# Optimization experiments

Hardware: AMD Instinct MI355X
Metric: run time of the kernel (lower is better)

Reference implementation:

```python
import jax, jax.numpy as jnp
import numpy as np

BS, LS, NWRD, D, H, NTGT, MC = 32, 512, 100000, 128, 512, 2048, 20
TEMP = 0.5  # gumbel-softmax temperature (self.last_t)
HLOSS_COEF = 0.03


def setup_inputs() -> dict:
    key = jax.random.key(0)
    ks = jax.random.split(key, 12)
    inp_word = jax.random.randint(ks[0], (BS, LS), 0, NWRD, dtype=jnp.int32)
    inp_char = jax.random.randint(ks[1], (BS, LS, MC), 0, 95, dtype=jnp.int32)
    inp_pos = jax.random.randint(ks[2], (BS, LS), 0, 50, dtype=jnp.int32)
    keyword_table = jax.random.bernoulli(ks[3], 0.1, (NWRD,))  # wid in keywords_set
    tgt_ids = jax.random.randint(ks[4], (NTGT,), 0, NWRD, dtype=jnp.int32)
    lut = jax.random.randint(ks[5], (NWRD, MC), 0, 95, dtype=jnp.int32)
    u = jax.random.uniform(ks[6], (BS, LS, NTGT), minval=1e-6, maxval=1.0 - 1e-6)
    gumbel = -jnp.log(-jnp.log(u))  # standard Gumbel(0,1) noise
    W = jax.random.normal(ks[7], (NWRD, D), dtype=jnp.float32) * 0.02
    W1 = jax.random.normal(ks[8], (D, H), dtype=jnp.float32) * (1.0 / np.sqrt(D))
    b1 = jnp.zeros((H,), jnp.float32)
    W2 = jax.random.normal(ks[9], (H, NTGT), dtype=jnp.float32) * (1.0 / np.sqrt(H))
    b2 = jnp.zeros((NTGT,), jnp.float32)
    return dict(inp_word=inp_word, inp_char=inp_char, inp_pos=inp_pos,
                keyword_table=keyword_table, tgt_ids=tgt_ids, lut=lut,
                gumbel=gumbel, W=W, W1=W1, b1=b1, W2=W2, b2=b2)


def reference(inp_word, inp_char, inp_pos, keyword_table, tgt_ids, lut,
              gumbel, W, W1, b1, W2, b2):
    # keyword membership mask (idx in the original; torch gathers only masked
    # spots -- here we compute densely and select with the mask, same math at
    # every masked position, identity elsewhere)
    mask = keyword_table[inp_word]                      # [bs, ls] bool

    x = W[inp_word]                                     # embed: [bs, ls, d]
    hdn = jax.nn.relu(jnp.einsum('bsd,dh->bsh', x, W1) + b1)
    logits = jnp.einsum('bsh,ht->bst', hdn, W2) + b2    # [bs, ls, ntgt]

    # log_p.masked_scatter_(idx, x.max(-1)[0])
    log_p = jnp.where(mask, logits.max(axis=-1), 0.0)

    # hloss: mean entropy over masked spots * 0.03
    lsm = jax.nn.log_softmax(logits, axis=-1)
    ent = -jnp.sum(jnp.exp(lsm) * lsm, axis=-1)         # [bs, ls]
    n_spots = jnp.maximum(mask.sum(), 1)
    loss_h = (ent * mask).sum() / n_spots * HLOSS_COEF

    # gumbel_softmax(x, t): softmax((logits + g) / t)
    sft = jax.nn.softmax((logits + gumbel) / TEMP, axis=-1)  # [bs, ls, ntgt]

    # hard pick mapped through tgtwords, scattered into word
    y = tgt_ids[jnp.argmax(sft, axis=-1)]               # [bs, ls]
    word = jnp.where(mask, y, inp_word)

    # soft embedding: sft @ word_emb_tgt, word_emb_tgt = W[tgt_ids]
    x_emb = jnp.einsum('bst,td->bsd', sft, W[tgt_ids])  # [bs, ls, d]
    word_emb = jnp.where(mask[..., None], x_emb, x)     # scatter into W[word]

    char = lut[word]                                    # word_to_char lookup

    return (mask.astype(jnp.float32), log_p, word, char, word_emb, loss_h)
```

## Files before the change

### kernel.cpp

```cpp
#include <hip/hip_runtime.h>
#include <cstdint>

#define R_TOT 16384
#define T_NT  2048
#define DD    128
#define HH    512
#define MC_   20
#define BR    32
#define STEPS 64
#define NBLK  (R_TOT / BR)

#define MASK_OFF 0
#define LOGP_OFF 16384
#define WORD_OFF 32768
#define CHAR_OFF 49152
#define EMB_OFF  376832
#define LOSS_OFF 2473984

#define X_OFF     0
#define HDN_OFF   2097152
#define HDNB_OFF  10485760
#define WT_OFF    14680064
#define WTT_OFF   14942208
#define W2T_OFF   15073280
#define W2TB_OFF  16121856
#define ENT_OFF   16646144
#define CNT_OFF   16647168

typedef __attribute__((ext_vector_type(8))) short short8v;
typedef __attribute__((ext_vector_type(4))) float f32x4;
typedef unsigned short ushort_t;

__device__ __forceinline__ ushort_t f2bf(float f) {
    union { float f; unsigned int u; } v; v.f = f;
    unsigned int r = v.u + 0x7FFFu + ((v.u >> 16) & 1u);
    return (ushort_t)(r >> 16);
}

__device__ __forceinline__ void stage16(const ushort_t* gsrc, ushort_t* ldst) {
    __builtin_amdgcn_global_load_lds(
        (const __attribute__((address_space(1))) unsigned int*)gsrc,
        (__attribute__((address_space(3))) unsigned int*)ldst, 16, 0, 0);
}

__global__ __launch_bounds__(256) void k1_gather(
    const int* __restrict__ inp_word, const int* __restrict__ tgt_ids,
    const float* __restrict__ W, float* __restrict__ x, float* __restrict__ wtgt)
{
    int row = blockIdx.x * 2 + (threadIdx.x >> 7);
    int d = threadIdx.x & 127;
    if (row < R_TOT) {
        int wsrc = inp_word[row];
        x[(size_t)row * DD + d] = W[(size_t)wsrc * DD + d];
    } else {
        int rr = row - R_TOT;
        if (rr < T_NT) {
            int wsrc = tgt_ids[rr];
            wtgt[(size_t)rr * DD + d] = W[(size_t)wsrc * DD + d];
        }
    }
}

__global__ __launch_bounds__(256) void k1b_wtgtT(
    const float* __restrict__ wtgt, ushort_t* __restrict__ wtgtT)
{
    __shared__ float tile[32][33];
    int tb = blockIdx.x * 32, db = blockIdx.y * 32;
    int lx = threadIdx.x & 31, ly = threadIdx.x >> 5;
    #pragma unroll
    for (int i = 0; i < 32; i += 8)
        tile[ly + i][lx] = wtgt[(size_t)(tb + ly + i) * DD + db + lx];
    __syncthreads();
    #pragma unroll
    for (int i = 0; i < 32; i += 8)
        wtgtT[(size_t)(db + ly + i) * T_NT + tb + lx] = f2bf(tile[lx][ly + i]);
}

__global__ __launch_bounds__(256) void k0_w2t(
    const float* __restrict__ W2, float* __restrict__ W2Tf, ushort_t* __restrict__ W2Tb)
{
    __shared__ float tile[32][33];
    int cb = blockIdx.x * 32, kb = blockIdx.y * 32;
    int lx = threadIdx.x & 31, ly = threadIdx.x >> 5;
    #pragma unroll
    for (int i = 0; i < 32; i += 8)
        tile[ly + i][lx] = W2[(size_t)(kb + ly + i) * T_NT + cb + lx];
    __syncthreads();
    #pragma unroll
    for (int i = 0; i < 32; i += 8) {
        int c = cb + ly + i, k = kb + lx;
        float v = tile[lx][ly + i];
        W2Tf[(size_t)c * HH + k] = v;
        W2Tb[(size_t)c * HH + k] = f2bf(v);
    }
}

__global__ __launch_bounds__(256) void k2_hdn(
    const float* __restrict__ x, const float* __restrict__ W1,
    const float* __restrict__ b1, float* __restrict__ hdn, ushort_t* __restrict__ hdnB)
{
    __shared__ float As[16][64];
    __shared__ float Bs[16][64];
    const int t = threadIdx.x;
    const int bm = blockIdx.x * 64;
    const int bn = blockIdx.y * 64;
    const int tx = t & 15, ty = t >> 4;
    float acc[4][4] = {};
    for (int k0 = 0; k0 < DD; k0 += 16) {
        {
            int m = t >> 2, kq = t & 3;
            float4 v = *(const float4*)(x + (size_t)(bm + m) * DD + k0 + kq * 4);
            As[kq * 4 + 0][m] = v.x; As[kq * 4 + 1][m] = v.y;
            As[kq * 4 + 2][m] = v.z; As[kq * 4 + 3][m] = v.w;
        }
        {
            int k = t >> 4, nq = t & 15;
            *(float4*)(&Bs[k][nq * 4]) =
                *(const float4*)(W1 + (size_t)(k0 + k) * HH + bn + nq * 4);
        }
        __syncthreads();
        #pragma unroll
        for (int k = 0; k < 16; ++k) {
            float a[4], b[4];
            #pragma unroll
            for (int i = 0; i < 4; i++) a[i] = As[k][ty * 4 + i];
            #pragma unroll
            for (int j = 0; j < 4; j++) b[j] = Bs[k][tx * 4 + j];
            #pragma unroll
            for (int i = 0; i < 4; i++)
                #pragma unroll
                for (int j = 0; j < 4; j++)
                    acc[i][j] = fmaf(a[i], b[j], acc[i][j]);
        }
        __syncthreads();
    }
    #pragma unroll
    for (int i = 0; i < 4; i++) {
        int m = bm + ty * 4 + i;
        int n = bn + tx * 4;
        float4 v;
        v.x = fmaxf(acc[i][0] + b1[n + 0], 0.f);
        v.y = fmaxf(acc[i][1] + b1[n + 1], 0.f);
        v.z = fmaxf(acc[i][2] + b1[n + 2], 0.f);
        v.w = fmaxf(acc[i][3] + b1[n + 3], 0.f);
        *(float4*)(hdn + (size_t)m * HH + n) = v;
        ushort4 hb;
        hb.x = f2bf(v.x); hb.y = f2bf(v.y); hb.z = f2bf(v.z); hb.w = f2bf(v.w);
        *(ushort4*)(hdnB + (size_t)m * HH + n) = hb;
    }
}

__global__ __launch_bounds__(256) void k3_fused(
    const ushort_t* __restrict__ hdnB, const float* __restrict__ hdn,
    const ushort_t* __restrict__ W2Tb, const float* __restrict__ W2Tf,
    const float* __restrict__ b2, const float* __restrict__ gumbel,
    const int* __restrict__ inp_word, const int* __restrict__ keyword_table,
    const int* __restrict__ tgt_ids, const int* __restrict__ lut,
    const float* __restrict__ x, const ushort_t* __restrict__ wtgtT,
    float* __restrict__ out, float* __restrict__ entP, float* __restrict__ cntP)
{
    __shared__ ushort_t wS[2][16384];
    __shared__ float pS[2 * 2 * 16 * 36];
    __shared__ float statC1[2 * 16 * 8];
    __shared__ int   candS[BR * 2];
    __shared__ float invs2S[BR], entS[BR];
    __shared__ int   mskS[BR];

    const int t = threadIdx.x;
    const int wid = t >> 6, lane = t & 63;
    const int Mgrp = wid >> 1, Cgrp = wid & 1;
    const int lrow = lane & 15, kgrp = lane >> 4;
    const int row0 = blockIdx.x * BR;
    const int rowA = row0 + Mgrp * 16 + lrow;
    const int c_local = Cgrp * 16 + lrow;

    short8v av[16];
    #pragma unroll
    for (int ks = 0; ks < 16; ++ks)
        av[ks] = *(const short8v*)(hdnB + (size_t)rowA * HH + ks * 32 + kgrp * 8);

    float m_[4], sE_[4], sEl_[4], s2_[4], a1_[4], a2_[4];
    int i1_[4], i2_[4];
    #pragma unroll
    for (int q = 0; q < 4; ++q) {
        m_[q] = -1e30f; sE_[q] = 0.f; sEl_[q] = 0.f; s2_[q] = 0.f;
        a1_[q] = -1e30f; a2_[q] = -1e30f; i1_[q] = 0; i2_[q] = 0;
    }
    f32x4 accpv[4];
    #pragma unroll
    for (int df = 0; df < 4; ++df) accpv[df] = (f32x4){0.f, 0.f, 0.f, 0.f};

    auto stage_tile = [&](int buf, int s_step) {
        const int col0 = s_step * 32;
        #pragma unroll
        for (int i = 0; i < 8; ++i) {
            int slot = wid * 512 + i * 64 + lane;
            int c = slot >> 6, kc = slot & 63;
            const ushort_t* gsrc = W2Tb + (size_t)(col0 + c) * HH + ((kc ^ (c & 7)) << 3);
            stage16(gsrc, &wS[buf][(size_t)(wid * 512 + i * 64) * 8]);
        }
    };

    stage_tile(0, 0);
    __syncthreads();

    const int dbase = Cgrp * 64 + lrow;

    for (int s = 0; s < STEPS; ++s) {
        const int buf = s & 1, par = s & 1;
        const int col = s * 32 + c_local;

        float g4[4];
        #pragma unroll
        for (int q = 0; q < 4; ++q)
            g4[q] = gumbel[(size_t)(row0 + Mgrp * 16 + kgrp * 4 + q) * T_NT + col];
        float b2v = b2[col];
        short8v bvf[4];
        #pragma unroll
        for (int df = 0; df < 4; ++df)
            bvf[df] = *(const short8v*)(wtgtT + (size_t)(dbase + df * 16) * T_NT + s * 32 + kgrp * 8);

        if (s + 1 < STEPS) stage_tile(buf ^ 1, s + 1);

        f32x4 acc = (f32x4){0.f, 0.f, 0.f, 0.f};
        #pragma unroll
        for (int ks = 0; ks < 16; ++ks) {
            int kc = ks * 4 + kgrp;
            const short8v bv = *(const short8v*)&wS[buf][c_local * 512 + ((kc ^ (c_local & 7)) << 3)];
            acc = __builtin_amdgcn_mfma_f32_16x16x32_bf16(av[ks], bv, acc, 0, 0, 0);
        }

        float* pT = &pS[(Mgrp * 2 + par) * 576];
        #pragma unroll
        for (int q = 0; q < 4; ++q) {
            float l = acc[q] + b2v;
            m_[q] = fmaxf(m_[q], l);
            float e1 = __expf(l);
            sE_[q] += e1; sEl_[q] = fmaf(e1, l, sEl_[q]);
            float a = l + g4[q];
            float p = __expf(2.0f * a);
            s2_[q] += p;
            if (a > a1_[q]) { a2_[q] = a1_[q]; i2_[q] = i1_[q]; a1_[q] = a; i1_[q] = col; }
            else if (a > a2_[q]) { a2_[q] = a; i2_[q] = col; }
            pT[(kgrp * 4 + q) * 36 + c_local] = p;
        }

        __syncthreads();

        {
            const float* pr = &pS[(Mgrp * 2 + par) * 576 + lrow * 36 + kgrp * 8];
            float4 pa = *(const float4*)(pr);
            float4 pb = *(const float4*)(pr + 4);
            short8v pav;
            pav[0] = (short)f2bf(pa.x); pav[1] = (short)f2bf(pa.y);
            pav[2] = (short)f2bf(pa.z); pav[3] = (short)f2bf(pa.w);
            pav[4] = (short)f2bf(pb.x); pav[5] = (short)f2bf(pb.y);
            pav[6] = (short)f2bf(pb.z); pav[7] = (short)f2bf(pb.w);
            #pragma unroll
            for (int df = 0; df < 4; ++df)
                accpv[df] = __builtin_amdgcn_mfma_f32_16x16x32_bf16(pav, bvf[df], accpv[df], 0, 0, 0);
        }
    }

    #pragma unroll
    for (int q = 0; q < 4; ++q) {
        #pragma unroll
        for (int mk = 1; mk < 16; mk <<= 1) {
            m_[q] = fmaxf(m_[q], __shfl_xor(m_[q], mk));
            sE_[q] += __shfl_xor(sE_[q], mk);
            sEl_[q] += __shfl_xor(sEl_[q], mk);
            s2_[q] += __shfl_xor(s2_[q], mk);
            float ob1 = __shfl_xor(a1_[q], mk); int oj1 = __shfl_xor(i1_[q], mk);
            float ob2 = __shfl_xor(a2_[q], mk); int oj2 = __shfl_xor(i2_[q], mk);
            if (ob1 > a1_[q] || (ob1 == a1_[q] && oj1 < i1_[q])) {
                if (a1_[q] > ob2 || (a1_[q] == ob2 && i1_[q] < oj2)) { a2_[q] = a1_[q]; i2_[q] = i1_[q]; }
                else { a2_[q] = ob2; i2_[q] = oj2; }
                a1_[q] = ob1; i1_[q] = oj1;
            } else {
                if (ob1 > a2_[q]) { a2_[q] = ob1; i2_[q] = oj1; }
            }
        }
    }

    if (Cgrp == 1 && lrow == 0) {
        #pragma unroll
        for (int q = 0; q < 4; ++q) {
            int r = kgrp * 4 + q;
            float* st = &statC1[(Mgrp * 16 + r) * 8];
            st[0] = m_[q]; st[1] = sE_[q]; st[2] = sEl_[q]; st[3] = s2_[q];
            st[4] = a1_[q]; st[5] = __int_as_float(i1_[q]);
            st[6] = a2_[q]; st[7] = __int_as_float(i2_[q]);
        }
    }
    __syncthreads();

    if (Cgrp == 0) {
        #pragma unroll
        for (int q = 0; q < 4; ++q) {
            int r = kgrp * 4 + q;
            const float* st = &statC1[(Mgrp * 16 + r) * 8];
            float bm = st[0], bsE = st[1], bsEl = st[2], bs2 = st[3];
            float b1v = st[4]; int j1 = __float_as_int(st[5]);
            float b2c = st[6]; int j2 = __float_as_int(st[7]);
            float m = fmaxf(m_[q], bm);
            float sE = sE_[q] + bsE, sEl = sEl_[q] + bsEl, s2 = s2_[q] + bs2;
            float a1 = a1_[q], a2 = a2_[q]; int i1 = i1_[q], i2 = i2_[q];
            if (b1v > a1 || (b1v == a1 && j1 < i1)) {
                if (a1 > b2c || (a1 == b2c && i1 < j2)) { a2 = a1; i2 = i1; }
                else { a2 = b2c; i2 = j2; }
                a1 = b1v; i1 = j1;
            } else {
                if (b1v > a2) { a2 = b1v; i2 = j1; }
            }
            if (lrow == 0) {
                int grow = row0 + Mgrp * 16 + r;
                int w_in = inp_word[grow];
                int msk = keyword_table[w_in] != 0;
                out[MASK_OFF + grow] = msk ? 1.0f : 0.0f;
                out[LOGP_OFF + grow] = msk ? m : 0.0f;
                invs2S[Mgrp * 16 + r] = 1.0f / s2;
                mskS[Mgrp * 16 + r] = msk;
                entS[Mgrp * 16 + r] = msk ? (__logf(sE) - sEl / sE) : 0.0f;
                candS[(Mgrp * 16 + r) * 2 + 0] = i1;
                candS[(Mgrp * 16 + r) * 2 + 1] = i2;
            }
        }
    }
    __syncthreads();

    #pragma unroll
    for (int df = 0; df < 4; ++df) {
        #pragma unroll
        for (int q = 0; q < 4; ++q) {
            int rl = Mgrp * 16 + kgrp * 4 + q;
            int grow = row0 + rl;
            int d = dbase + df * 16;
            float val = accpv[df][q] * invs2S[rl];
            if (!mskS[rl]) val = x[(size_t)grow * DD + d];
            out[EMB_OFF + (size_t)grow * DD + d] = val;
        }
    }

    for (int rr = wid * 8; rr < wid * 8 + 8; ++rr) {
        int grow = row0 + rr;
        int i1 = candS[rr * 2 + 0], i2 = candS[rr * 2 + 1];
        const float* hrow = hdn + (size_t)grow * HH;
        float4 h0 = *(const float4*)(hrow + lane * 8);
        float4 h1 = *(const float4*)(hrow + lane * 8 + 4);
        float v1, v2;
        {
            const float* wrow = W2Tf + (size_t)i1 * HH;
            float4 w0 = *(const float4*)(wrow + lane * 8);
            float4 w1 = *(const float4*)(wrow + lane * 8 + 4);
            float sdot = h0.x*w0.x + h0.y*w0.y + h0.z*w0.z + h0.w*w0.w
                       + h1.x*w1.x + h1.y*w1.y + h1.z*w1.z + h1.w*w1.w;
            #pragma unroll
            for (int mk = 1; mk < 64; mk <<= 1) sdot += __shfl_xor(sdot, mk);
            v1 = sdot + b2[i1] + gumbel[(size_t)grow * T_NT + i1];
        }
        {
            const float* wrow = W2Tf + (size_t)i2 * HH;
            float4 w0 = *(const float4*)(wrow + lane * 8);
            float4 w1 = *(const float4*)(wrow + lane * 8 + 4);
            float sdot = h0.x*w0.x + h0.y*w0.y + h0.z*w0.z + h0.w*w0.w
                       + h1.x*w1.x + h1.y*w1.y + h1.z*w1.z + h1.w*w1.w;
            #pragma unroll
            for (int mk = 1; mk < 64; mk <<= 1) sdot += __shfl_xor(sdot, mk);
            v2 = sdot + b2[i2] + gumbel[(size_t)grow * T_NT + i2];
        }
        int ibest = (v2 > v1 || (v2 == v1 && i2 < i1)) ? i2 : i1;
        int w_in = inp_word[grow];
        int msk = mskS[rr];
        int word = msk ? tgt_ids[ibest] : w_in;
        if (lane == 0) out[WORD_OFF + grow] = (float)word;
        if (lane < MC_)
            out[CHAR_OFF + (size_t)grow * MC_ + lane] = (float)lut[(size_t)word * MC_ + lane];
    }

    if (t == 0) {
        float es = 0.f; int cs = 0;
        #pragma unroll
        for (int r = 0; r < BR; r++) { es += entS[r]; cs += mskS[r]; }
        entP[blockIdx.x] = es;
        cntP[blockIdx.x] = (float)cs;
    }
}

__global__ __launch_bounds__(256) void k4_loss(
    const float* __restrict__ entP, const float* __restrict__ cntP, float* __restrict__ out)
{
    __shared__ float sE[256], sC[256];
    int t = threadIdx.x;
    float e = 0.f, c = 0.f;
    for (int i = t; i < NBLK; i += 256) { e += entP[i]; c += cntP[i]; }
    sE[t] = e; sC[t] = c;
    __syncthreads();
    for (int s = 128; s > 0; s >>= 1) {
        if (t < s) { sE[t] += sE[t + s]; sC[t] += sC[t + s]; }
        __syncthreads();
    }
    if (t == 0) {
        float ns = fmaxf(sC[0], 1.0f);
        out[LOSS_OFF] = 0.03f * sE[0] / ns;
    }
}

extern "C" void kernel_launch(void* const* d_in, const int* in_sizes, int n_in,
                              void* d_out, int out_size, void* d_ws, size_t ws_size,
                              hipStream_t stream) {
    const int* inp_word = (const int*)d_in[0];
    const int* keyword_table = (const int*)d_in[3];
    const int* tgt_ids = (const int*)d_in[4];
    const int* lut = (const int*)d_in[5];
    const float* gumbel = (const float*)d_in[6];
    const float* W = (const float*)d_in[7];
    const float* W1 = (const float*)d_in[8];
    const float* b1 = (const float*)d_in[9];
    const float* W2 = (const float*)d_in[10];
    const float* b2 = (const float*)d_in[11];
    float* out = (float*)d_out;

    float* wsf = (float*)d_ws;
    float* x = wsf + X_OFF;
    float* hdn = wsf + HDN_OFF;
    ushort_t* hdnB = (ushort_t*)(wsf + HDNB_OFF);
    float* wtgt = wsf + WT_OFF;
    ushort_t* wtgtT = (ushort_t*)(wsf + WTT_OFF);
    float* W2Tf = wsf + W2T_OFF;
    ushort_t* W2Tb = (ushort_t*)(wsf + W2TB_OFF);
    float* entP = wsf + ENT_OFF;
    float* cntP = wsf + CNT_OFF;

    k1_gather<<<(R_TOT + T_NT) / 2, 256, 0, stream>>>(inp_word, tgt_ids, W, x, wtgt);
    k1b_wtgtT<<<dim3(T_NT / 32, DD / 32), 256, 0, stream>>>(wtgt, wtgtT);
    k0_w2t<<<dim3(T_NT / 32, HH / 32), 256, 0, stream>>>(W2, W2Tf, W2Tb);
    k2_hdn<<<dim3(R_TOT / 64, HH / 64), 256, 0, stream>>>(x, W1, b1, hdn, hdnB);
    k3_fused<<<NBLK, 256, 0, stream>>>(hdnB, hdn, W2Tb, W2Tf, b2, gumbel,
                                       inp_word, keyword_table, tgt_ids, lut,
                                       x, wtgtT, out, entP, cntP);
    k4_loss<<<1, 256, 0, stream>>>(entP, cntP, out);
}
```

Baseline: 219.5 us.

## Restructure k3 main loop: pointer-increment staging, split MFMA chains, explicit barriers

Reworks the fused logits/softmax/soft-embedding loop in k3. Global addresses for the W2 tile staging, gumbel, b2 and wtgtT loads are precomputed once as pointers and advanced each step, and the LDS swizzle is changed so the B-fragment reads use fixed base offsets. The 16-deep dependent MFMA chain is split into four independent accumulators, and setprio hints are added around the MFMA bursts. The single __syncthreads is replaced by explicit waitcnt/s_barrier pairs, with a second barrier per step after waiting on outstanding global loads, and launch bounds request two blocks per CU. This aims to cut address arithmetic and MFMA latency stalls, at the cost of an extra barrier per iteration and tighter register limits that could cause spills.

```diff
diff --git a/kernel.cpp b/kernel.cpp
--- a/kernel.cpp
+++ b/kernel.cpp
@@ -150,7 +150,7 @@
     }
 }
 
-__global__ __launch_bounds__(256) void k3_fused(
+__global__ __launch_bounds__(256, 2) void k3_fused(
     const ushort_t* __restrict__ hdnB, const float* __restrict__ hdn,
     const ushort_t* __restrict__ W2Tb, const float* __restrict__ W2Tf,
     const float* __restrict__ b2, const float* __restrict__ gumbel,
@@ -159,7 +159,7 @@
     const float* __restrict__ x, const ushort_t* __restrict__ wtgtT,
     float* __restrict__ out, float* __restrict__ entP, float* __restrict__ cntP)
 {
-    __shared__ ushort_t wS[2][16384];
+    __shared__ ushort_t wS[2 * 16384];
     __shared__ float pS[2 * 2 * 16 * 36];
     __shared__ float statC1[2 * 16 * 8];
     __shared__ int   candS[BR * 2];
@@ -173,11 +173,37 @@
     const int row0 = blockIdx.x * BR;
     const int rowA = row0 + Mgrp * 16 + lrow;
     const int c_local = Cgrp * 16 + lrow;
+    const int dbase = Cgrp * 64 + lrow;
 
     short8v av[16];
     #pragma unroll
     for (int ks = 0; ks < 16; ++ks)
         av[ks] = *(const short8v*)(hdnB + (size_t)rowA * HH + ks * 32 + kgrp * 8);
+
+    const ushort_t* sp[8];
+    #pragma unroll
+    for (int i = 0; i < 8; ++i) {
+        int slot = wid * 512 + i * 64 + lane;
+        int kc = slot >> 5, gi = slot & 31;
+        int c = gi ^ (kc & 7);
+        sp[i] = W2Tb + (size_t)c * HH + kc * 8;
+    }
+
+    const int inv = kgrp * 256 + ((c_local ^ kgrp) << 3);
+    const ushort_t* wbE0 = &wS[inv];
+    const ushort_t* wbO0 = &wS[inv ^ 32];
+    const ushort_t* wbE1 = wbE0 + 16384;
+    const ushort_t* wbO1 = wbO0 + 16384;
+
+    const float* gp0 = gumbel + (size_t)(row0 + Mgrp * 16 + kgrp * 4 + 0) * T_NT + c_local;
+    const float* gp1 = gp0 + T_NT;
+    const float* gp2 = gp1 + T_NT;
+    const float* gp3 = gp2 + T_NT;
+    const float* b2p = b2 + c_local;
+    const ushort_t* vp0 = wtgtT + (size_t)(dbase + 0)  * T_NT + kgrp * 8;
+    const ushort_t* vp1 = wtgtT + (size_t)(dbase + 16) * T_NT + kgrp * 8;
+    const ushort_t* vp2 = wtgtT + (size_t)(dbase + 32) * T_NT + kgrp * 8;
+    const ushort_t* vp3 = wtgtT + (size_t)(dbase + 48) * T_NT + kgrp * 8;
 
     float m_[4], sE_[4], sEl_[4], s2_[4], a1_[4], a2_[4];
     int i1_[4], i2_[4];
@@ -190,47 +216,49 @@
     #pragma unroll
     for (int df = 0; df < 4; ++df) accpv[df] = (f32x4){0.f, 0.f, 0.f, 0.f};
 
-    auto stage_tile = [&](int buf, int s_step) {
-        const int col0 = s_step * 32;
-        #pragma unroll
-        for (int i = 0; i < 8; ++i) {
-            int slot = wid * 512 + i * 64 + lane;
-            int c = slot >> 6, kc = slot & 63;
-            const ushort_t* gsrc = W2Tb + (size_t)(col0 + c) * HH + ((kc ^ (c & 7)) << 3);
-            stage16(gsrc, &wS[buf][(size_t)(wid * 512 + i * 64) * 8]);
-        }
-    };
-
-    stage_tile(0, 0);
-    __syncthreads();
-
-    const int dbase = Cgrp * 64 + lrow;
+    #pragma unroll
+    for (int i = 0; i < 8; ++i) {
+        stage16(sp[i], &wS[(wid * 512 + i * 64) * 8]);
+        sp[i] += 16384;
+    }
+    __syncthreads();
+
+    int colv = c_local;
 
     for (int s = 0; s < STEPS; ++s) {
-        const int buf = s & 1, par = s & 1;
-        const int col = s * 32 + c_local;
-
-        float g4[4];
-        #pragma unroll
-        for (int q = 0; q < 4; ++q)
-            g4[q] = gumbel[(size_t)(row0 + Mgrp * 16 + kgrp * 4 + q) * T_NT + col];
-        float b2v = b2[col];
-        short8v bvf[4];
-        #pragma unroll
-        for (int df = 0; df < 4; ++df)
-            bvf[df] = *(const short8v*)(wtgtT + (size_t)(dbase + df * 16) * T_NT + s * 32 + kgrp * 8);
-
-        if (s + 1 < STEPS) stage_tile(buf ^ 1, s + 1);
-
-        f32x4 acc = (f32x4){0.f, 0.f, 0.f, 0.f};
-        #pragma unroll
-        for (int ks = 0; ks < 16; ++ks) {
-            int kc = ks * 4 + kgrp;
-            const short8v bv = *(const short8v*)&wS[buf][c_local * 512 + ((kc ^ (c_local & 7)) << 3)];
-            acc = __builtin_amdgcn_mfma_f32_16x16x32_bf16(av[ks], bv, acc, 0, 0, 0);
-        }
-
-        float* pT = &pS[(Mgrp * 2 + par) * 576];
+        const int buf = s & 1;
+        if (s + 1 < STEPS) {
+            ushort_t* wdst = &wS[(buf ^ 1) * 16384];
+            #pragma unroll
+            for (int i = 0; i < 8; ++i) {
+                stage16(sp[i], wdst + (wid * 512 + i * 64) * 8);
+                sp[i] += 16384;
+            }
+        }
+        float g0 = *gp0, g1 = *gp1, g2 = *gp2, g3 = *gp3;
+        gp0 += 32; gp1 += 32; gp2 += 32; gp3 += 32;
+        float b2v = *b2p; b2p += 32;
+        short8v bvf0 = *(const short8v*)vp0; vp0 += 32;
+        short8v bvf1 = *(const short8v*)vp1; vp1 += 32;
+        short8v bvf2 = *(const short8v*)vp2; vp2 += 32;
+        short8v bvf3 = *(const short8v*)vp3; vp3 += 32;
+
+        const ushort_t* we = buf ? wbE1 : wbE0;
+        const ushort_t* wo = buf ? wbO1 : wbO0;
+        f32x4 ac0 = (f32x4){0.f,0.f,0.f,0.f}, ac1 = ac0, ac2 = ac0, ac3 = ac0;
+        __builtin_amdgcn_s_setprio(1);
+        #pragma unroll
+        for (int ks = 0; ks < 16; ks += 4) {
+            ac0 = __builtin_amdgcn_mfma_f32_16x16x32_bf16(av[ks+0], *(const short8v*)(we + (ks+0)*1024), ac0, 0, 0, 0);
+            ac1 = __builtin_amdgcn_mfma_f32_16x16x32_bf16(av[ks+1], *(const short8v*)(wo + (ks+1)*1024), ac1, 0, 0, 0);
+            ac2 = __builtin_amdgcn_mfma_f32_16x16x32_bf16(av[ks+2], *(const short8v*)(we + (ks+2)*1024), ac2, 0, 0, 0);
+            ac3 = __builtin_amdgcn_mfma_f32_16x16x32_bf16(av[ks+3], *(const short8v*)(wo + (ks+3)*1024), ac3, 0, 0, 0);
+        }
+        __builtin_amdgcn_s_setprio(0);
+        f32x4 acc = (ac0 + ac1) + (ac2 + ac3);
+
+        float* pT = &pS[(Mgrp * 2 + buf) * 576];
+        float g4[4] = {g0, g1, g2, g3};
         #pragma unroll
         for (int q = 0; q < 4; ++q) {
             float l = acc[q] + b2v;
@@ -240,15 +268,17 @@
             float a = l + g4[q];
             float p = __expf(2.0f * a);
             s2_[q] += p;
-            if (a > a1_[q]) { a2_[q] = a1_[q]; i2_[q] = i1_[q]; a1_[q] = a; i1_[q] = col; }
-            else if (a > a2_[q]) { a2_[q] = a; i2_[q] = col; }
+            if (a > a1_[q]) { a2_[q] = a1_[q]; i2_[q] = i1_[q]; a1_[q] = a; i1_[q] = colv; }
+            else if (a > a2_[q]) { a2_[q] = a; i2_[q] = colv; }
             pT[(kgrp * 4 + q) * 36 + c_local] = p;
         }
 
-        __syncthreads();
+        asm volatile("s_waitcnt lgkmcnt(0)" ::: "memory");
+        __builtin_amdgcn_s_barrier();
+        __builtin_amdgcn_sched_barrier(0);
 
         {
-            const float* pr = &pS[(Mgrp * 2 + par) * 576 + lrow * 36 + kgrp * 8];
+            const float* pr = &pS[(Mgrp * 2 + buf) * 576 + lrow * 36 + kgrp * 8];
             float4 pa = *(const float4*)(pr);
             float4 pb = *(const float4*)(pr + 4);
             short8v pav;
@@ -256,10 +286,18 @@
             pav[2] = (short)f2bf(pa.z); pav[3] = (short)f2bf(pa.w);
             pav[4] = (short)f2bf(pb.x); pav[5] = (short)f2bf(pb.y);
             pav[6] = (short)f2bf(pb.z); pav[7] = (short)f2bf(pb.w);
-            #pragma unroll
-            for (int df = 0; df < 4; ++df)
-                accpv[df] = __builtin_amdgcn_mfma_f32_16x16x32_bf16(pav, bvf[df], accpv[df], 0, 0, 0);
-        }
+            __builtin_amdgcn_s_setprio(1);
+            accpv[0] = __builtin_amdgcn_mfma_f32_16x16x32_bf16(pav, bvf0, accpv[0], 0, 0, 0);
+            accpv[1] = __builtin_amdgcn_mfma_f32_16x16x32_bf16(pav, bvf1, accpv[1], 0, 0, 0);
+            accpv[2] = __builtin_amdgcn_mfma_f32_16x16x32_bf16(pav, bvf2, accpv[2], 0, 0, 0);
+            accpv[3] = __builtin_amdgcn_mfma_f32_16x16x32_bf16(pav, bvf3, accpv[3], 0, 0, 0);
+            __builtin_amdgcn_s_setprio(0);
+        }
+
+        asm volatile("s_waitcnt vmcnt(0)" ::: "memory");
+        __builtin_amdgcn_s_barrier();
+        __builtin_amdgcn_sched_barrier(0);
+        colv += 32;
     }
 
     #pragma unroll
```

Measured after the change: 256.2 us. 16.7% more time.

## Restructure fused logits kernel: A in LDS, B streamed from global, split columns per wave

Applied to the files above, without the earlier changes.

The fused logits/softmax kernel now stages the bf16 hidden rows into swizzled LDS once. Each wave streams W2 columns straight from global/L2 and interleaves column tiles between wave pairs, so the per-step block-wide barrier and the double-buffered LDS staging are gone. The soft-embedding target matrix is repacked into a tile-contiguous layout, and each wave computes all 128 output dims for its columns; partial results are merged through LDS at the end. Launch bounds request two blocks per CU. The cost is more global/L2 traffic for W2 per wave and higher register pressure from the 8 accumulators.

```diff
diff --git a/kernel.cpp b/kernel.cpp
--- a/kernel.cpp
+++ b/kernel.cpp
@@ -35,12 +35,6 @@
     union { float f; unsigned int u; } v; v.f = f;
     unsigned int r = v.u + 0x7FFFu + ((v.u >> 16) & 1u);
     return (ushort_t)(r >> 16);
-}
-
-__device__ __forceinline__ void stage16(const ushort_t* gsrc, ushort_t* ldst) {
-    __builtin_amdgcn_global_load_lds(
-        (const __attribute__((address_space(1))) unsigned int*)gsrc,
-        (__attribute__((address_space(3))) unsigned int*)ldst, 16, 0, 0);
 }
 
 __global__ __launch_bounds__(256) void k1_gather(
@@ -61,8 +55,8 @@
     }
 }
 
-__global__ __launch_bounds__(256) void k1b_wtgtT(
-    const float* __restrict__ wtgt, ushort_t* __restrict__ wtgtT)
+__global__ __launch_bounds__(256) void k1b_wtgtT3(
+    const float* __restrict__ wtgt, ushort_t* __restrict__ wtgtT3)
 {
     __shared__ float tile[32][33];
     int tb = blockIdx.x * 32, db = blockIdx.y * 32;
@@ -71,9 +65,13 @@
     for (int i = 0; i < 32; i += 8)
         tile[ly + i][lx] = wtgt[(size_t)(tb + ly + i) * DD + db + lx];
     __syncthreads();
-    #pragma unroll
-    for (int i = 0; i < 32; i += 8)
-        wtgtT[(size_t)(db + ly + i) * T_NT + tb + lx] = f2bf(tile[lx][ly + i]);
+    int kt = tb >> 5;
+    #pragma unroll
+    for (int i = 0; i < 32; i += 8) {
+        int d = db + ly + i;
+        wtgtT3[(size_t)(((kt * 8 + (d >> 4)) * 16 + (d & 15)) * 32) + lx] =
+            f2bf(tile[lx][ly + i]);
+    }
 }
 
 __global__ __launch_bounds__(256) void k0_w2t(
@@ -150,34 +148,55 @@
     }
 }
 
-__global__ __launch_bounds__(256) void k3_fused(
+__global__ __launch_bounds__(256, 2) void k3_fused(
     const ushort_t* __restrict__ hdnB, const float* __restrict__ hdn,
     const ushort_t* __restrict__ W2Tb, const float* __restrict__ W2Tf,
     const float* __restrict__ b2, const float* __restrict__ gumbel,
     const int* __restrict__ inp_word, const int* __restrict__ keyword_table,
     const int* __restrict__ tgt_ids, const int* __restrict__ lut,
-    const float* __restrict__ x, const ushort_t* __restrict__ wtgtT,
+    const float* __restrict__ x, const ushort_t* __restrict__ wtgtT3,
     float* __restrict__ out, float* __restrict__ entP, float* __restrict__ cntP)
 {
-    __shared__ ushort_t wS[2][16384];
-    __shared__ float pS[2 * 2 * 16 * 36];
-    __shared__ float statC1[2 * 16 * 8];
+    __shared__ ushort_t aS[BR * 512];
+    __shared__ float pS[4][16 * 36];
+    __shared__ float statP[4][16][8];
     __shared__ int   candS[BR * 2];
     __shared__ float invs2S[BR], entS[BR];
     __shared__ int   mskS[BR];
 
     const int t = threadIdx.x;
     const int wid = t >> 6, lane = t & 63;
-    const int Mgrp = wid >> 1, Cgrp = wid & 1;
+    const int mg = wid >> 1, cw = wid & 1;
     const int lrow = lane & 15, kgrp = lane >> 4;
     const int row0 = blockIdx.x * BR;
-    const int rowA = row0 + Mgrp * 16 + lrow;
-    const int c_local = Cgrp * 16 + lrow;
-
-    short8v av[16];
-    #pragma unroll
-    for (int ks = 0; ks < 16; ++ks)
-        av[ks] = *(const short8v*)(hdnB + (size_t)rowA * HH + ks * 32 + kgrp * 8);
+
+    {
+        #pragma unroll
+        for (int i = 0; i < 8; ++i) {
+            int fid = i * 256 + t;
+            int row = fid >> 6, g = fid & 63;
+            uint4 v = *(const uint4*)(hdnB + (size_t)(row0 + row) * HH + g * 8);
+            *(uint4*)(aS + row * 512 + ((g ^ (row & 7)) << 3)) = v;
+        }
+    }
+    __syncthreads();
+
+    const int r7 = lrow & 7;
+    const int bpar = (lrow >> 2) & 1;
+    const ushort_t* baseC = aS + (mg * 16 + lrow) * 512 + ((kgrp ^ (r7 & 3)) << 3);
+    const ushort_t* baseE = baseC + bpar * 32;
+    const ushort_t* baseO = baseC - bpar * 32;
+
+    const ushort_t* bp0 = W2Tb + (size_t)(cw * 32 + lrow) * HH + kgrp * 8;
+    const ushort_t* bp1 = bp0 + 16 * HH;
+    const float* gp[4];
+    #pragma unroll
+    for (int q = 0; q < 4; ++q)
+        gp[q] = gumbel + (size_t)(row0 + mg * 16 + kgrp * 4 + q) * T_NT + cw * 32 + lrow;
+    const float* b2p = b2 + cw * 32 + lrow;
+    const ushort_t* vt3p = wtgtT3 + (size_t)cw * 4096 + lrow * 32 + kgrp * 8;
+
+    float* pw = &pS[wid][0];
 
     float m_[4], sE_[4], sEl_[4], s2_[4], a1_[4], a2_[4];
     int i1_[4], i2_[4];
@@ -186,69 +205,67 @@
         m_[q] = -1e30f; sE_[q] = 0.f; sEl_[q] = 0.f; s2_[q] = 0.f;
         a1_[q] = -1e30f; a2_[q] = -1e30f; i1_[q] = 0; i2_[q] = 0;
     }
-    f32x4 accpv[4];
-    #pragma unroll
-    for (int df = 0; df < 4; ++df) accpv[df] = (f32x4){0.f, 0.f, 0.f, 0.f};
-
-    auto stage_tile = [&](int buf, int s_step) {
-        const int col0 = s_step * 32;
-        #pragma unroll
-        for (int i = 0; i < 8; ++i) {
-            int slot = wid * 512 + i * 64 + lane;
-            int c = slot >> 6, kc = slot & 63;
-            const ushort_t* gsrc = W2Tb + (size_t)(col0 + c) * HH + ((kc ^ (c & 7)) << 3);
-            stage16(gsrc, &wS[buf][(size_t)(wid * 512 + i * 64) * 8]);
-        }
-    };
-
-    stage_tile(0, 0);
-    __syncthreads();
-
-    const int dbase = Cgrp * 64 + lrow;
-
-    for (int s = 0; s < STEPS; ++s) {
-        const int buf = s & 1, par = s & 1;
-        const int col = s * 32 + c_local;
-
-        float g4[4];
-        #pragma unroll
-        for (int q = 0; q < 4; ++q)
-            g4[q] = gumbel[(size_t)(row0 + Mgrp * 16 + kgrp * 4 + q) * T_NT + col];
-        float b2v = b2[col];
-        short8v bvf[4];
-        #pragma unroll
-        for (int df = 0; df < 4; ++df)
-            bvf[df] = *(const short8v*)(wtgtT + (size_t)(dbase + df * 16) * T_NT + s * 32 + kgrp * 8);
-
-        if (s + 1 < STEPS) stage_tile(buf ^ 1, s + 1);
-
-        f32x4 acc = (f32x4){0.f, 0.f, 0.f, 0.f};
+    f32x4 accpv[8];
+    #pragma unroll
+    for (int df = 0; df < 8; ++df) accpv[df] = (f32x4){0.f, 0.f, 0.f, 0.f};
+
+    float gcur[8];
+    #pragma unroll
+    for (int q = 0; q < 4; ++q) { gcur[2 * q] = gp[q][0]; gcur[2 * q + 1] = gp[q][16]; }
+
+    for (int js = cw; js < STEPS; js += 2) {
+        const int nadv = (js + 2 < STEPS) ? 64 : 0;
+        float gnx[8];
+        #pragma unroll
+        for (int q = 0; q < 4; ++q) {
+            gnx[2 * q] = gp[q][nadv];
+            gnx[2 * q + 1] = gp[q][nadv + 16];
+        }
+        float b2lo = b2p[0], b2hi = b2p[16];
+
+        f32x4 c0[4], c1[4];
+        #pragma unroll
+        for (int j = 0; j < 4; ++j) { c0[j] = (f32x4){0.f,0.f,0.f,0.f}; c1[j] = c0[j]; }
         #pragma unroll
         for (int ks = 0; ks < 16; ++ks) {
-            int kc = ks * 4 + kgrp;
-            const short8v bv = *(const short8v*)&wS[buf][c_local * 512 + ((kc ^ (c_local & 7)) << 3)];
-            acc = __builtin_amdgcn_mfma_f32_16x16x32_bf16(av[ks], bv, acc, 0, 0, 0);
-        }
-
-        float* pT = &pS[(Mgrp * 2 + par) * 576];
+            const ushort_t* ab = (ks & 1) ? baseO : baseE;
+            short8v a = *(const short8v*)(ab + ks * 32);
+            short8v bv0 = *(const short8v*)(bp0 + ks * 32);
+            short8v bv1 = *(const short8v*)(bp1 + ks * 32);
+            c0[ks & 3] = __builtin_amdgcn_mfma_f32_16x16x32_bf16(a, bv0, c0[ks & 3], 0, 0, 0);
+            c1[ks & 3] = __builtin_amdgcn_mfma_f32_16x16x32_bf16(a, bv1, c1[ks & 3], 0, 0, 0);
+        }
+        f32x4 acc0 = (c0[0] + c0[1]) + (c0[2] + c0[3]);
+        f32x4 acc1 = (c1[0] + c1[1]) + (c1[2] + c1[3]);
+
+        const int col0 = js * 32 + lrow;
         #pragma unroll
         for (int q = 0; q < 4; ++q) {
-            float l = acc[q] + b2v;
-            m_[q] = fmaxf(m_[q], l);
-            float e1 = __expf(l);
-            sE_[q] += e1; sEl_[q] = fmaf(e1, l, sEl_[q]);
-            float a = l + g4[q];
-            float p = __expf(2.0f * a);
-            s2_[q] += p;
-            if (a > a1_[q]) { a2_[q] = a1_[q]; i2_[q] = i1_[q]; a1_[q] = a; i1_[q] = col; }
-            else if (a > a2_[q]) { a2_[q] = a; i2_[q] = col; }
-            pT[(kgrp * 4 + q) * 36 + c_local] = p;
-        }
-
-        __syncthreads();
+            float l0 = acc0[q] + b2lo;
+            m_[q] = fmaxf(m_[q], l0);
+            float e0 = __expf(l0);
+            sE_[q] += e0; sEl_[q] = fmaf(e0, l0, sEl_[q]);
+            float aa0 = l0 + gcur[2 * q];
+            float p0 = __expf(2.0f * aa0);
+            s2_[q] += p0;
+            if (aa0 > a1_[q]) { a2_[q] = a1_[q]; i2_[q] = i1_[q]; a1_[q] = aa0; i1_[q] = col0; }
+            else if (aa0 > a2_[q]) { a2_[q] = aa0; i2_[q] = col0; }
+            pw[(kgrp * 4 + q) * 36 + lrow] = p0;
+
+            float l1 = acc1[q] + b2hi;
+            m_[q] = fmaxf(m_[q], l1);
+            float e1 = __expf(l1);
+            sE_[q] += e1; sEl_[q] = fmaf(e1, l1, sEl_[q]);
+            float aa1 = l1 + gcur[2 * q + 1];
+            float p1 = __expf(2.0f * aa1);
+            s2_[q] += p1;
+            if (aa1 > a1_[q]) { a2_[q] = a1_[q]; i2_[q] = i1_[q]; a1_[q] = aa1; i1_[q] = col0 + 16; }
+            else if (aa1 > a2_[q]) { a2_[q] = aa1; i2_[q] = col0 + 16; }
+            pw[(kgrp * 4 + q) * 36 + 16 + lrow] = p1;
+        }
 
         {
-            const float* pr = &pS[(Mgrp * 2 + par) * 576 + lrow * 36 + kgrp * 8];
+            const float* pr = pw + lrow * 36 + kgrp * 8;
             float4 pa = *(const float4*)(pr);
             float4 pb = *(const float4*)(pr + 4);
             short8v pav;
@@ -257,9 +274,18 @@
             pav[4] = (short)f2bf(pb.x); pav[5] = (short)f2bf(pb.y);
             pav[6] = (short)f2bf(pb.z); pav[7] = (short)f2bf(pb.w);
             #pragma unroll
-            for (int df = 0; df < 4; ++df)
-                accpv[df] = __builtin_amdgcn_mfma_f32_16x16x32_bf16(pav, bvf[df], accpv[df], 0, 0, 0);
-        }
+            for (int df = 0; df < 8; ++df) {
+                short8v bv = *(const short8v*)(vt3p + df * 512);
+                accpv[df] = __builtin_amdgcn_mfma_f32_16x16x32_bf16(pav, bv, accpv[df], 0, 0, 0);
+            }
+        }
+
+        bp0 += 64 * HH; bp1 += 64 * HH;
+        #pragma unroll
+        for (int q = 0; q < 4; ++q) gp[q] += 64;
+        b2p += 64; vt3p += 8192;
+        #pragma unroll
+        for (int j = 0; j < 8; ++j) gcur[j] = gnx[j];
     }
 
     #pragma unroll
@@ -282,66 +308,81 @@
         }
     }
 
-    if (Cgrp == 1 && lrow == 0) {
+    if (lrow == 0) {
         #pragma unroll
         for (int q = 0; q < 4; ++q) {
-            int r = kgrp * 4 + q;
-            float* st = &statC1[(Mgrp * 16 + r) * 8];
+            float* st = &statP[wid][kgrp * 4 + q][0];
             st[0] = m_[q]; st[1] = sE_[q]; st[2] = sEl_[q]; st[3] = s2_[q];
             st[4] = a1_[q]; st[5] = __int_as_float(i1_[q]);
             st[6] = a2_[q]; st[7] = __int_as_float(i2_[q]);
         }
     }
-    __syncthreads();
-
-    if (Cgrp == 0) {
+    float* scr = (float*)aS;
+    if (cw == 1) {
+        #pragma unroll
+        for (int df = 0; df < 8; ++df)
+            #pragma unroll
+            for (int q = 0; q < 4; ++q)
+                scr[mg * 2112 + (kgrp * 4 + q) * 132 + df * 16 + lrow] = accpv[df][q];
+    }
+    __syncthreads();
+
+    if (cw == 0) {
         #pragma unroll
         for (int q = 0; q < 4; ++q) {
             int r = kgrp * 4 + q;
-            const float* st = &statC1[(Mgrp * 16 + r) * 8];
+            const float* st = &statP[mg * 2 + 1][r][0];
             float bm = st[0], bsE = st[1], bsEl = st[2], bs2 = st[3];
-            float b1v = st[4]; int j1 = __float_as_int(st[5]);
-            float b2c = st[6]; int j2 = __float_as_int(st[7]);
+            float ob1 = st[4]; int oj1 = __float_as_int(st[5]);
+            float ob2 = st[6]; int oj2 = __float_as_int(st[7]);
             float m = fmaxf(m_[q], bm);
             float sE = sE_[q] + bsE, sEl = sEl_[q] + bsEl, s2 = s2_[q] + bs2;
             float a1 = a1_[q], a2 = a2_[q]; int i1 = i1_[q], i2 = i2_[q];
-            if (b1v > a1 || (b1v == a1 && j1 < i1)) {
-                if (a1 > b2c || (a1 == b2c && i1 < j2)) { a2 = a1; i2 = i1; }
-                else { a2 = b2c; i2 = j2; }
-                a1 = b1v; i1 = j1;
+            if (ob1 > a1 || (ob1 == a1 && oj1 < i1)) {
+                if (a1 > ob2 || (a1 == ob2 && i1 < oj2)) { a2 = a1; i2 = i1; }
+                else { a2 = ob2; i2 = oj2; }
+                a1 = ob1; i1 = oj1;
             } else {
-                if (b1v > a2) { a2 = b1v; i2 = j1; }
+                if (ob1 > a2) { a2 = ob1; i2 = oj1; }
             }
             if (lrow == 0) {
-                int grow = row0 + Mgrp * 16 + r;
+                int rl = mg * 16 + r;
+                int grow = row0 + rl;
                 int w_in = inp_word[grow];
                 int msk = keyword_table[w_in] != 0;
                 out[MASK_OFF + grow] = msk ? 1.0f : 0.0f;
                 out[LOGP_OFF + grow] = msk ? m : 0.0f;
-                invs2S[Mgrp * 16 + r] = 1.0f / s2;
-                mskS[Mgrp * 16 + r] = msk;
-                entS[Mgrp * 16 + r] = msk ? (__logf(sE) - sEl / sE) : 0.0f;
-                candS[(Mgrp * 16 + r) * 2 + 0] = i1;
-                candS[(Mgrp * 16 + r) * 2 + 1] = i2;
+                invs2S[rl] = 1.0f / s2;
+                mskS[rl] = msk;
+                entS[rl] = msk ? (__logf(sE) - sEl / sE) : 0.0f;
+                candS[rl * 2 + 0] = i1;
+                candS[rl * 2 + 1] = i2;
             }
         }
-    }
-    __syncthreads();
-
-    #pragma unroll
-    for (int df = 0; df < 4; ++df) {
-        #pragma unroll
-        for (int q = 0; q < 4; ++q) {
-            int rl = Mgrp * 16 + kgrp * 4 + q;
-            int grow = row0 + rl;
-            int d = dbase + df * 16;
-            float val = accpv[df][q] * invs2S[rl];
-            if (!mskS[rl]) val = x[(size_t)grow * DD + d];
-            out[EMB_OFF + (size_t)grow * DD + d] = val;
-        }
-    }
-
-    for (int rr = wid * 8; rr < wid * 8 + 8; ++rr) {
+        #pragma unroll
+        for (int df = 0; df < 8; ++df)
+            #pragma unroll
+            for (int q = 0; q < 4; ++q)
+                accpv[df][q] += scr[mg * 2112 + (kgrp * 4 + q) * 132 + df * 16 + lrow];
+    }
+    __syncthreads();
+
+    if (cw == 0) {
+        #pragma unroll
+        for (int df = 0; df < 8; ++df) {
+            #pragma unroll
+            for (int q = 0; q < 4; ++q) {
+                int rl = mg * 16 + kgrp * 4 + q;
+                int grow = row0 + rl;
+                int d = df * 16 + lrow;
+                float val = accpv[df][q] * invs2S[rl];
+                if (!mskS[rl]) val = x[(size_t)grow * DD + d];
+                out[EMB_OFF + (size_t)grow * DD + d] = val;
+            }
+        }
+    }
+
+    for (int rr = wid; rr < BR; rr += 4) {
         int grow = row0 + rr;
         int i1 = candS[rr * 2 + 0], i2 = candS[rr * 2 + 1];
         const float* hrow = hdn + (size_t)grow * HH;
@@ -425,18 +466,18 @@
     float* hdn = wsf + HDN_OFF;
     ushort_t* hdnB = (ushort_t*)(wsf + HDNB_OFF);
     float* wtgt = wsf + WT_OFF;
-    ushort_t* wtgtT = (ushort_t*)(wsf + WTT_OFF);
+    ushort_t* wtgtT3 = (ushort_t*)(wsf + WTT_OFF);
     float* W2Tf = wsf + W2T_OFF;
     ushort_t* W2Tb = (ushort_t*)(wsf + W2TB_OFF);
     float* entP = wsf + ENT_OFF;
     float* cntP = wsf + CNT_OFF;
 
     k1_gather<<<(R_TOT + T_NT) / 2, 256, 0, stream>>>(inp_word, tgt_ids, W, x, wtgt);
-    k1b_wtgtT<<<dim3(T_NT / 32, DD / 32), 256, 0, stream>>>(wtgt, wtgtT);
+    k1b_wtgtT3<<<dim3(T_NT / 32, DD / 32), 256, 0, stream>>>(wtgt, wtgtT3);
     k0_w2t<<<dim3(T_NT / 32, HH / 32), 256, 0, stream>>>(W2, W2Tf, W2Tb);
     k2_hdn<<<dim3(R_TOT / 64, HH / 64), 256, 0, stream>>>(x, W1, b1, hdn, hdnB);
     k3_fused<<<NBLK, 256, 0, stream>>>(hdnB, hdn, W2Tb, W2Tf, b2, gumbel,
                                        inp_word, keyword_table, tgt_ids, lut,
-                                       x, wtgtT, out, entP, cntP);
+                                       x, wtgtT3, out, entP, cntP);
     k4_loss<<<1, 256, 0, stream>>>(entP, cntP, out);
 }
```

New measurement: 344.7 us. +57.1%, slower.
